# Kernel optimization log

Measured on AMD Instinct MI355X. Metric: run time of the kernel, lower is better.

Reference implementation:

```python
import jax, jax.numpy as jnp
import numpy as np

UNITS = 1024
OMEGA = np.float32(2.0 * np.pi / UNITS)  # Hopf rotation frequency tied to units
MU = np.float32(1.0)                      # bifurcation parameter (the stop-gradient ones)


def _hopf_act(z_prev, z_i):
    # Hopf normal-form activation: z_i + ((mu - |z_i|^2) + i*omega) * z_i
    r2 = z_i.real * z_i.real + z_i.imag * z_i.imag  # float32 [B,U]
    coef = jax.lax.complex(MU - r2, jnp.full_like(r2, OMEGA))
    return z_i + coef * z_i


def setup_inputs() -> dict:
    key = jax.random.key(0)
    ks = jax.random.split(key, 8)
    B, T, U = 64, 512, UNITS
    ws = np.float32(1.0 / np.sqrt(2.0 * U))  # glorot-ish scale for complex weights
    return {
        "x_real": jax.random.normal(ks[0], (B, T, U), dtype=jnp.float32),
        "x_imag": jax.random.normal(ks[1], (B, T, U), dtype=jnp.float32),
        "A_real": jax.random.normal(ks[2], (U, U), dtype=jnp.float32) * ws,
        "A_imag": jax.random.normal(ks[3], (U, U), dtype=jnp.float32) * ws,
        "B_real": jax.random.normal(ks[4], (U, U), dtype=jnp.float32) * ws,
        "B_imag": jax.random.normal(ks[5], (U, U), dtype=jnp.float32) * ws,
        "z0_real": jax.random.normal(ks[6], (B, U), dtype=jnp.float32) * 0.1,
        "z0_imag": jax.random.normal(ks[7], (B, U), dtype=jnp.float32) * 0.1,
    }


def reference(x_real, x_imag, A_real, A_imag, B_real, B_imag, z0_real, z0_imag):
    x = jax.lax.complex(x_real, x_imag)      # [B,T,U] complex64
    A = jax.lax.complex(A_real, A_imag)      # [U,U]
    Bw = jax.lax.complex(B_real, B_imag)     # [U,U]
    z0 = jax.lax.complex(z0_real, z0_imag)   # [B,U]

    def step(z, x_t):
        # z_i = (z @ A + x @ B) / 2 ; new state is z_i, output is Hopf activation
        z_i = (jnp.matmul(z, A) + jnp.matmul(x_t, Bw)) * np.complex64(0.5)
        y_t = _hopf_act(z, z_i)
        return z_i, y_t

    xs = jnp.swapaxes(x, 0, 1)               # [T,B,U]
    _, ys = jax.lax.scan(step, z0, xs)       # ys: [T,B,U]
    ys = jnp.swapaxes(ys, 0, 1)              # [B,T,U]
    # return real/imag stacked so output is float32 [B,T,U,2]
    return jnp.stack([ys.real, ys.imag], axis=-1)
```

## Files before the change

kernel.cpp:

```cpp
#include <hip/hip_runtime.h>
#include <hip/hip_bf16.h>


#define U_DIM 1024
#define T_STEPS 512
#define B_DIM 64
#define CHUNK 16
#define NCH 32
#define R_ROWS 2048

typedef __bf16 bf16;
typedef __attribute__((ext_vector_type(8))) __bf16 bf16x8;
typedef __attribute__((ext_vector_type(4))) float floatx4;
typedef __attribute__((ext_vector_type(8))) float floatx8;
typedef __attribute__((ext_vector_type(2))) float floatx2;
typedef __attribute__((ext_vector_type(4))) int intx4;

static constexpr float OMEGA_F = 0.006135923151542565f;

__global__ __launch_bounds__(256) void wtrans_kernel(
    const float* __restrict__ a0, const float* __restrict__ a1,
    const float* __restrict__ a2, const float* __restrict__ a3,
    bf16* __restrict__ d0, bf16* __restrict__ d1,
    bf16* __restrict__ d2, bf16* __restrict__ d3)
{
  __shared__ bf16 tile[32][33];
  const float* src;
  bf16* dst;
  switch (blockIdx.z) {
    case 0: src = a0; dst = d0; break;
    case 1: src = a1; dst = d1; break;
    case 2: src = a2; dst = d2; break;
    default: src = a3; dst = d3; break;
  }
  const int tx = threadIdx.x;
  const int ty = threadIdx.y;
  const int k0 = blockIdx.x * 32;
  const int n0 = blockIdx.y * 32;
#pragma unroll
  for (int i = 0; i < 4; ++i) {
    int k = k0 + ty + i * 8;
    tile[ty + i * 8][tx] = (bf16)(0.5f * src[(size_t)k * U_DIM + n0 + tx]);
  }
  __syncthreads();
#pragma unroll
  for (int i = 0; i < 4; ++i) {
    int n = n0 + ty + i * 8;
    dst[(size_t)n * U_DIM + k0 + tx] = tile[tx][ty + i * 8];
  }
}

__global__ __launch_bounds__(256) void zinit2_kernel(
    const float* __restrict__ zr, const float* __restrict__ zi,
    bf16* __restrict__ br, bf16* __restrict__ bi)
{
  size_t idx = (size_t)blockIdx.x * 256 + threadIdx.x;
  int row = (int)(idx >> 10);
  int col = (int)(idx & 1023);
  float vr = 0.f, vi = 0.f;
  if (row < 128) {
    int b = row & 63;
    vr = zr[(size_t)b * U_DIM + col];
    vi = zi[(size_t)b * U_DIM + col];
  }
  br[idx] = (bf16)vr;
  bi[idx] = (bf16)vi;
}

__global__ __launch_bounds__(512) void phase1_kernel(
    const float* __restrict__ Xr, const float* __restrict__ Xi,
    const bf16* __restrict__ Wr, const bf16* __restrict__ Wi,
    float* __restrict__ out)
{
  const int lane = threadIdx.x & 63;
  const int wave = threadIdx.x >> 6;
  const int m0 = blockIdx.x * 32;
  const int n0 = blockIdx.y * 512 + wave * 64;
  const int l16 = lane & 15;
  const int kq = (lane >> 4) * 8;

  floatx4 accr[2][4], acci[2][4];
#pragma unroll
  for (int ms = 0; ms < 2; ++ms)
#pragma unroll
    for (int ns = 0; ns < 4; ++ns) {
      accr[ms][ns] = (floatx4){0.f, 0.f, 0.f, 0.f};
      acci[ms][ns] = (floatx4){0.f, 0.f, 0.f, 0.f};
    }

  const float* xr0 = Xr + (size_t)(m0 + l16) * U_DIM + kq;
  const float* xi0 = Xi + (size_t)(m0 + l16) * U_DIM + kq;
  const bf16* wr0 = Wr + (size_t)(n0 + l16) * U_DIM + kq;
  const bf16* wi0 = Wi + (size_t)(n0 + l16) * U_DIM + kq;

#pragma unroll 2
  for (int kb = 0; kb < U_DIM; kb += 32) {
    bf16x8 ar[2], ai[2], nai[2];
#pragma unroll
    for (int ms = 0; ms < 2; ++ms) {
      floatx8 fr = *(const floatx8*)(xr0 + (size_t)ms * 16 * U_DIM + kb);
      floatx8 fi = *(const floatx8*)(xi0 + (size_t)ms * 16 * U_DIM + kb);
      ar[ms] = __builtin_convertvector(fr, bf16x8);
      ai[ms] = __builtin_convertvector(fi, bf16x8);
      intx4 v = __builtin_bit_cast(intx4, ai[ms]);
      v = v ^ (int)0x80008000u;
      nai[ms] = __builtin_bit_cast(bf16x8, v);
    }
    bf16x8 br[4], bi[4];
#pragma unroll
    for (int ns = 0; ns < 4; ++ns) {
      br[ns] = *(const bf16x8*)(wr0 + (size_t)ns * 16 * U_DIM + kb);
      bi[ns] = *(const bf16x8*)(wi0 + (size_t)ns * 16 * U_DIM + kb);
    }
#pragma unroll
    for (int ms = 0; ms < 2; ++ms)
#pragma unroll
      for (int ns = 0; ns < 4; ++ns) {
        accr[ms][ns] = __builtin_amdgcn_mfma_f32_16x16x32_bf16(ar[ms], br[ns], accr[ms][ns], 0, 0, 0);
        accr[ms][ns] = __builtin_amdgcn_mfma_f32_16x16x32_bf16(nai[ms], bi[ns], accr[ms][ns], 0, 0, 0);
        acci[ms][ns] = __builtin_amdgcn_mfma_f32_16x16x32_bf16(ar[ms], bi[ns], acci[ms][ns], 0, 0, 0);
        acci[ms][ns] = __builtin_amdgcn_mfma_f32_16x16x32_bf16(ai[ms], br[ns], acci[ms][ns], 0, 0, 0);
      }
  }

  const int rb = (lane >> 4) * 4;
#pragma unroll
  for (int ms = 0; ms < 2; ++ms)
#pragma unroll
    for (int ns = 0; ns < 4; ++ns)
#pragma unroll
      for (int r = 0; r < 4; ++r) {
        int row = m0 + ms * 16 + rb + r;
        int col = n0 + ns * 16 + l16;
        floatx2 v = {accr[ms][ns][r], acci[ms][ns][r]};
        *(floatx2*)(out + ((size_t)row * U_DIM + col) * 2) = v;
      }
}

__global__ __launch_bounds__(256) void bigstep_kernel(
    const bf16* __restrict__ Zr_in, const bf16* __restrict__ Zi_in,
    const bf16* __restrict__ Wr, const bf16* __restrict__ Wi,
    bf16* __restrict__ Zr_out, bf16* __restrict__ Zi_out,
    float* __restrict__ out, int s, int write_y)
{
  const int lane = threadIdx.x & 63;
  const int wave = threadIdx.x >> 6;
  const int m0 = blockIdx.x * 128 + wave * 32;
  const int n0 = blockIdx.y * 64;
  const int l16 = lane & 15;
  const int kq = (lane >> 4) * 8;

  floatx4 accr[2][4], acci[2][4];
#pragma unroll
  for (int ms = 0; ms < 2; ++ms)
#pragma unroll
    for (int ns = 0; ns < 4; ++ns) {
      accr[ms][ns] = (floatx4){0.f, 0.f, 0.f, 0.f};
      acci[ms][ns] = (floatx4){0.f, 0.f, 0.f, 0.f};
    }

  const bf16* zr0 = Zr_in + (size_t)(m0 + l16) * U_DIM + kq;
  const bf16* zi0 = Zi_in + (size_t)(m0 + l16) * U_DIM + kq;
  const bf16* wr0 = Wr + (size_t)(n0 + l16) * U_DIM + kq;
  const bf16* wi0 = Wi + (size_t)(n0 + l16) * U_DIM + kq;

#pragma unroll 4
  for (int kb = 0; kb < U_DIM; kb += 32) {
    bf16x8 ar[2], ai[2], nai[2];
#pragma unroll
    for (int ms = 0; ms < 2; ++ms) {
      ar[ms] = *(const bf16x8*)(zr0 + (size_t)ms * 16 * U_DIM + kb);
      ai[ms] = *(const bf16x8*)(zi0 + (size_t)ms * 16 * U_DIM + kb);
      intx4 v = __builtin_bit_cast(intx4, ai[ms]);
      v = v ^ (int)0x80008000u;
      nai[ms] = __builtin_bit_cast(bf16x8, v);
    }
    bf16x8 br[4], bi[4];
#pragma unroll
    for (int ns = 0; ns < 4; ++ns) {
      br[ns] = *(const bf16x8*)(wr0 + (size_t)ns * 16 * U_DIM + kb);
      bi[ns] = *(const bf16x8*)(wi0 + (size_t)ns * 16 * U_DIM + kb);
    }
#pragma unroll
    for (int ms = 0; ms < 2; ++ms)
#pragma unroll
      for (int ns = 0; ns < 4; ++ns) {
        accr[ms][ns] = __builtin_amdgcn_mfma_f32_16x16x32_bf16(ar[ms], br[ns], accr[ms][ns], 0, 0, 0);
        accr[ms][ns] = __builtin_amdgcn_mfma_f32_16x16x32_bf16(nai[ms], bi[ns], accr[ms][ns], 0, 0, 0);
        acci[ms][ns] = __builtin_amdgcn_mfma_f32_16x16x32_bf16(ar[ms], bi[ns], acci[ms][ns], 0, 0, 0);
        acci[ms][ns] = __builtin_amdgcn_mfma_f32_16x16x32_bf16(ai[ms], br[ns], acci[ms][ns], 0, 0, 0);
      }
  }

  const int rb = (lane >> 4) * 4;
#pragma unroll
  for (int ms = 0; ms < 2; ++ms)
#pragma unroll
    for (int ns = 0; ns < 4; ++ns)
#pragma unroll
      for (int r = 0; r < 4; ++r) {
        int row = m0 + ms * 16 + rb + r;
        int c = row >> 6;
        int b = row & 63;
        int t = c * CHUNK + s;
        int col = n0 + ns * 16 + l16;
        size_t o = (((size_t)b * T_STEPS + t) * U_DIM + col) * 2;
        floatx2 u = *(const floatx2*)(out + o);
        float zrv = accr[ms][ns][r] + u.x;
        float ziv = acci[ms][ns][r] + u.y;
        Zr_out[(size_t)row * U_DIM + col] = (bf16)zrv;
        Zi_out[(size_t)row * U_DIM + col] = (bf16)ziv;
        if (write_y) {
          float r2 = zrv * zrv + ziv * ziv;
          float cr = 2.0f - r2;
          floatx2 y = {cr * zrv - OMEGA_F * ziv, cr * ziv + OMEGA_F * zrv};
          *(floatx2*)(out + o) = y;
        }
      }
}

extern "C" void kernel_launch(void* const* d_in, const int* in_sizes, int n_in,
                              void* d_out, int out_size, void* d_ws, size_t ws_size,
                              hipStream_t stream)
{
  const float* Xr  = (const float*)d_in[0];
  const float* Xi  = (const float*)d_in[1];
  const float* Ar  = (const float*)d_in[2];
  const float* Ai  = (const float*)d_in[3];
  const float* Br  = (const float*)d_in[4];
  const float* Bi  = (const float*)d_in[5];
  const float* z0r = (const float*)d_in[6];
  const float* z0i = (const float*)d_in[7];
  float* out = (float*)d_out;

  char* ws = (char*)d_ws;
  const size_t WW = (size_t)U_DIM * U_DIM;
  const size_t SB = (size_t)(1 + NCH) * B_DIM * U_DIM;
  const size_t CHOFF = (size_t)B_DIM * U_DIM;
  bf16* Atr = (bf16*)ws;
  bf16* Ati = Atr + WW;
  bf16* Btr = Ati + WW;
  bf16* Bti = Btr + WW;
  bf16* S0r = Bti + WW;
  bf16* S0i = S0r + SB;
  bf16* S1r = S0i + SB;
  bf16* S1i = S1r + SB;

  (void)in_sizes; (void)n_in; (void)out_size; (void)ws_size;

  wtrans_kernel<<<dim3(32, 32, 4), dim3(32, 8), 0, stream>>>(
      Ar, Ai, Br, Bi, Atr, Ati, Btr, Bti);

  zinit2_kernel<<<dim3((unsigned)(SB / 256)), dim3(256), 0, stream>>>(
      z0r, z0i, S0r, S0i);

  phase1_kernel<<<dim3(1024, 2), dim3(512), 0, stream>>>(Xr, Xi, Btr, Bti, out);

  for (int s = 0; s < CHUNK; ++s) {
    const bf16 *ir_, *ii_;
    bf16 *or_, *oi_;
    if ((s & 1) == 0) { ir_ = S0r + CHOFF; ii_ = S0i + CHOFF; or_ = S1r + CHOFF; oi_ = S1i + CHOFF; }
    else              { ir_ = S1r + CHOFF; ii_ = S1i + CHOFF; or_ = S0r + CHOFF; oi_ = S0i + CHOFF; }
    bigstep_kernel<<<dim3(16, 16), dim3(256), 0, stream>>>(
        ir_, ii_, Atr, Ati, or_, oi_, out, s, 0);
  }

  for (int s = 0; s < CHUNK; ++s) {
    const bf16 *ir_, *ii_;
    bf16 *or_, *oi_;
    if (s == 0)       { ir_ = S0r;         ii_ = S0i;         or_ = S1r + CHOFF; oi_ = S1i + CHOFF; }
    else if (s & 1)   { ir_ = S1r + CHOFF; ii_ = S1i + CHOFF; or_ = S0r + CHOFF; oi_ = S0i + CHOFF; }
    else              { ir_ = S0r + CHOFF; ii_ = S0i + CHOFF; or_ = S1r + CHOFF; oi_ = S1i + CHOFF; }
    bigstep_kernel<<<dim3(16, 16), dim3(256), 0, stream>>>(
        ir_, ii_, Atr, Ati, or_, oi_, out, s, 1);
  }
}
```

Baseline: 3.598 ms.

## Tile input-projection GEMM through LDS and split-K the recurrent step kernel

The input projection kernel now stages 128x128 tiles of X (converted to bf16) and W through shared memory with register prefetch of the next K slice, giving each block much more operand reuse than the old per-wave direct global loads. The recurrent step kernel is restructured so the four waves each handle a quarter of K for a 32x64 output tile, with partial sums reduced through LDS by wave 0. This quadruples the grid of each step launch to fill more compute units. The cost is extra LDS traffic, barriers, and a serialized reduction and epilogue on one wave.

```diff
diff --git a/kernel.cpp b/kernel.cpp
--- a/kernel.cpp
+++ b/kernel.cpp
@@ -7,7 +7,6 @@
 #define B_DIM 64
 #define CHUNK 16
 #define NCH 32
-#define R_ROWS 2048
 
 typedef __bf16 bf16;
 typedef __attribute__((ext_vector_type(8))) __bf16 bf16x8;
@@ -67,41 +66,152 @@
   bi[idx] = (bf16)vi;
 }
 
-__global__ __launch_bounds__(512) void phase1_kernel(
+__global__ __launch_bounds__(256, 2) void phase1_kernel(
     const float* __restrict__ Xr, const float* __restrict__ Xi,
     const bf16* __restrict__ Wr, const bf16* __restrict__ Wi,
     float* __restrict__ out)
 {
-  const int lane = threadIdx.x & 63;
-  const int wave = threadIdx.x >> 6;
-  const int m0 = blockIdx.x * 32;
-  const int n0 = blockIdx.y * 512 + wave * 64;
+  __shared__ __align__(16) bf16 ldsA[2][4][128][8];
+  __shared__ __align__(16) bf16 ldsB[2][4][128][8];
+
+  const int t = threadIdx.x;
+  const int lane = t & 63;
+  const int wave = t >> 6;
+  const int wm = wave >> 1;
+  const int wn = wave & 1;
+  const int n0 = blockIdx.x * 128;
+  const int m0 = blockIdx.y * 128;
   const int l16 = lane & 15;
-  const int kq = (lane >> 4) * 8;
-
-  floatx4 accr[2][4], acci[2][4];
-#pragma unroll
-  for (int ms = 0; ms < 2; ++ms)
+  const int kqf = lane >> 4;
+
+  const int sm = t & 127;
+  const int skq = t >> 7;
+
+  floatx4 accr[4][4], acci[4][4];
+#pragma unroll
+  for (int ms = 0; ms < 4; ++ms)
 #pragma unroll
     for (int ns = 0; ns < 4; ++ns) {
       accr[ms][ns] = (floatx4){0.f, 0.f, 0.f, 0.f};
       acci[ms][ns] = (floatx4){0.f, 0.f, 0.f, 0.f};
     }
 
-  const float* xr0 = Xr + (size_t)(m0 + l16) * U_DIM + kq;
-  const float* xi0 = Xi + (size_t)(m0 + l16) * U_DIM + kq;
-  const bf16* wr0 = Wr + (size_t)(n0 + l16) * U_DIM + kq;
-  const bf16* wi0 = Wi + (size_t)(n0 + l16) * U_DIM + kq;
+  const float* xr_base = Xr + (size_t)(m0 + sm) * U_DIM;
+  const float* xi_base = Xi + (size_t)(m0 + sm) * U_DIM;
+  const bf16* wr_base = Wr + (size_t)(n0 + sm) * U_DIM;
+  const bf16* wi_base = Wi + (size_t)(n0 + sm) * U_DIM;
+
+  floatx8 pxr[2], pxi[2];
+  bf16x8 pwr[2], pwi[2];
+
+#define P1_LOADS(KB)                                        \
+  do {                                                      \
+    int ko0 = (KB) + skq * 8;                               \
+    int ko1 = ko0 + 16;                                     \
+    pxr[0] = *(const floatx8*)(xr_base + ko0);              \
+    pxi[0] = *(const floatx8*)(xi_base + ko0);              \
+    pwr[0] = *(const bf16x8*)(wr_base + ko0);               \
+    pwi[0] = *(const bf16x8*)(wi_base + ko0);               \
+    pxr[1] = *(const floatx8*)(xr_base + ko1);              \
+    pxi[1] = *(const floatx8*)(xi_base + ko1);              \
+    pwr[1] = *(const bf16x8*)(wr_base + ko1);               \
+    pwi[1] = *(const bf16x8*)(wi_base + ko1);               \
+  } while (0)
+
+  P1_LOADS(0);
+
+#pragma unroll 1
+  for (int kb = 0; kb < U_DIM; kb += 32) {
+    *(bf16x8*)&ldsA[0][skq][sm][0]     = __builtin_convertvector(pxr[0], bf16x8);
+    *(bf16x8*)&ldsA[1][skq][sm][0]     = __builtin_convertvector(pxi[0], bf16x8);
+    *(bf16x8*)&ldsB[0][skq][sm][0]     = pwr[0];
+    *(bf16x8*)&ldsB[1][skq][sm][0]     = pwi[0];
+    *(bf16x8*)&ldsA[0][skq + 2][sm][0] = __builtin_convertvector(pxr[1], bf16x8);
+    *(bf16x8*)&ldsA[1][skq + 2][sm][0] = __builtin_convertvector(pxi[1], bf16x8);
+    *(bf16x8*)&ldsB[0][skq + 2][sm][0] = pwr[1];
+    *(bf16x8*)&ldsB[1][skq + 2][sm][0] = pwi[1];
+    __syncthreads();
+
+    if (kb + 32 < U_DIM) P1_LOADS(kb + 32);
+
+    bf16x8 br_[4], bi_[4];
+#pragma unroll
+    for (int ns = 0; ns < 4; ++ns) {
+      int nrow = wn * 64 + ns * 16 + l16;
+      br_[ns] = *(const bf16x8*)&ldsB[0][kqf][nrow][0];
+      bi_[ns] = *(const bf16x8*)&ldsB[1][kqf][nrow][0];
+    }
+#pragma unroll
+    for (int ms = 0; ms < 4; ++ms) {
+      int mrow = wm * 64 + ms * 16 + l16;
+      bf16x8 a_r = *(const bf16x8*)&ldsA[0][kqf][mrow][0];
+      bf16x8 a_i = *(const bf16x8*)&ldsA[1][kqf][mrow][0];
+      intx4 v = __builtin_bit_cast(intx4, a_i);
+      v = v ^ (int)0x80008000u;
+      bf16x8 n_ai = __builtin_bit_cast(bf16x8, v);
+#pragma unroll
+      for (int ns = 0; ns < 4; ++ns) {
+        accr[ms][ns] = __builtin_amdgcn_mfma_f32_16x16x32_bf16(a_r,  br_[ns], accr[ms][ns], 0, 0, 0);
+        accr[ms][ns] = __builtin_amdgcn_mfma_f32_16x16x32_bf16(n_ai, bi_[ns], accr[ms][ns], 0, 0, 0);
+        acci[ms][ns] = __builtin_amdgcn_mfma_f32_16x16x32_bf16(a_r,  bi_[ns], acci[ms][ns], 0, 0, 0);
+        acci[ms][ns] = __builtin_amdgcn_mfma_f32_16x16x32_bf16(a_i,  br_[ns], acci[ms][ns], 0, 0, 0);
+      }
+    }
+    __syncthreads();
+  }
+#undef P1_LOADS
+
+  const int rb = (lane >> 4) * 4;
+#pragma unroll
+  for (int ms = 0; ms < 4; ++ms)
+#pragma unroll
+    for (int ns = 0; ns < 4; ++ns)
+#pragma unroll
+      for (int r = 0; r < 4; ++r) {
+        int row = m0 + wm * 64 + ms * 16 + rb + r;
+        int col = n0 + wn * 64 + ns * 16 + l16;
+        floatx2 v = {accr[ms][ns][r], acci[ms][ns][r]};
+        *(floatx2*)(out + ((size_t)row * U_DIM + col) * 2) = v;
+      }
+}
+
+__global__ __launch_bounds__(256, 3) void bigstep_kernel(
+    const bf16* __restrict__ Zr_in, const bf16* __restrict__ Zi_in,
+    const bf16* __restrict__ Wr, const bf16* __restrict__ Wi,
+    bf16* __restrict__ Zr_out, bf16* __restrict__ Zi_out,
+    float* __restrict__ out, int s, int write_y)
+{
+  __shared__ floatx2 hs[3][32 * 64];
+
+  const int lane = threadIdx.x & 63;
+  const int wave = threadIdx.x >> 6;
+  const int n0 = blockIdx.x * 64;
+  const int m0 = blockIdx.y * 32;
+  const int l16 = lane & 15;
+  const int kq = (lane >> 4) * 8;
+  const int kbase = wave * 256;
+
+  floatx4 accr[2][4], acci[2][4];
+#pragma unroll
+  for (int ms = 0; ms < 2; ++ms)
+#pragma unroll
+    for (int ns = 0; ns < 4; ++ns) {
+      accr[ms][ns] = (floatx4){0.f, 0.f, 0.f, 0.f};
+      acci[ms][ns] = (floatx4){0.f, 0.f, 0.f, 0.f};
+    }
+
+  const bf16* zr0 = Zr_in + (size_t)(m0 + l16) * U_DIM + kbase + kq;
+  const bf16* zi0 = Zi_in + (size_t)(m0 + l16) * U_DIM + kbase + kq;
+  const bf16* wr0 = Wr + (size_t)(n0 + l16) * U_DIM + kbase + kq;
+  const bf16* wi0 = Wi + (size_t)(n0 + l16) * U_DIM + kbase + kq;
 
 #pragma unroll 2
-  for (int kb = 0; kb < U_DIM; kb += 32) {
+  for (int kb = 0; kb < 256; kb += 32) {
     bf16x8 ar[2], ai[2], nai[2];
 #pragma unroll
     for (int ms = 0; ms < 2; ++ms) {
-      floatx8 fr = *(const floatx8*)(xr0 + (size_t)ms * 16 * U_DIM + kb);
-      floatx8 fi = *(const floatx8*)(xi0 + (size_t)ms * 16 * U_DIM + kb);
-      ar[ms] = __builtin_convertvector(fr, bf16x8);
-      ai[ms] = __builtin_convertvector(fi, bf16x8);
+      ar[ms] = *(const bf16x8*)(zr0 + (size_t)ms * 16 * U_DIM + kb);
+      ai[ms] = *(const bf16x8*)(zi0 + (size_t)ms * 16 * U_DIM + kb);
       intx4 v = __builtin_bit_cast(intx4, ai[ms]);
       v = v ^ (int)0x80008000u;
       nai[ms] = __builtin_bit_cast(bf16x8, v);
@@ -124,99 +234,51 @@
   }
 
   const int rb = (lane >> 4) * 4;
-#pragma unroll
-  for (int ms = 0; ms < 2; ++ms)
-#pragma unroll
-    for (int ns = 0; ns < 4; ++ns)
-#pragma unroll
-      for (int r = 0; r < 4; ++r) {
-        int row = m0 + ms * 16 + rb + r;
-        int col = n0 + ns * 16 + l16;
-        floatx2 v = {accr[ms][ns][r], acci[ms][ns][r]};
-        *(floatx2*)(out + ((size_t)row * U_DIM + col) * 2) = v;
-      }
-}
-
-__global__ __launch_bounds__(256) void bigstep_kernel(
-    const bf16* __restrict__ Zr_in, const bf16* __restrict__ Zi_in,
-    const bf16* __restrict__ Wr, const bf16* __restrict__ Wi,
-    bf16* __restrict__ Zr_out, bf16* __restrict__ Zi_out,
-    float* __restrict__ out, int s, int write_y)
-{
-  const int lane = threadIdx.x & 63;
-  const int wave = threadIdx.x >> 6;
-  const int m0 = blockIdx.x * 128 + wave * 32;
-  const int n0 = blockIdx.y * 64;
-  const int l16 = lane & 15;
-  const int kq = (lane >> 4) * 8;
-
-  floatx4 accr[2][4], acci[2][4];
-#pragma unroll
-  for (int ms = 0; ms < 2; ++ms)
-#pragma unroll
-    for (int ns = 0; ns < 4; ++ns) {
-      accr[ms][ns] = (floatx4){0.f, 0.f, 0.f, 0.f};
-      acci[ms][ns] = (floatx4){0.f, 0.f, 0.f, 0.f};
-    }
-
-  const bf16* zr0 = Zr_in + (size_t)(m0 + l16) * U_DIM + kq;
-  const bf16* zi0 = Zi_in + (size_t)(m0 + l16) * U_DIM + kq;
-  const bf16* wr0 = Wr + (size_t)(n0 + l16) * U_DIM + kq;
-  const bf16* wi0 = Wi + (size_t)(n0 + l16) * U_DIM + kq;
-
-#pragma unroll 4
-  for (int kb = 0; kb < U_DIM; kb += 32) {
-    bf16x8 ar[2], ai[2], nai[2];
-#pragma unroll
-    for (int ms = 0; ms < 2; ++ms) {
-      ar[ms] = *(const bf16x8*)(zr0 + (size_t)ms * 16 * U_DIM + kb);
-      ai[ms] = *(const bf16x8*)(zi0 + (size_t)ms * 16 * U_DIM + kb);
-      intx4 v = __builtin_bit_cast(intx4, ai[ms]);
-      v = v ^ (int)0x80008000u;
-      nai[ms] = __builtin_bit_cast(bf16x8, v);
-    }
-    bf16x8 br[4], bi[4];
-#pragma unroll
-    for (int ns = 0; ns < 4; ++ns) {
-      br[ns] = *(const bf16x8*)(wr0 + (size_t)ns * 16 * U_DIM + kb);
-      bi[ns] = *(const bf16x8*)(wi0 + (size_t)ns * 16 * U_DIM + kb);
-    }
+  if (wave != 0) {
 #pragma unroll
     for (int ms = 0; ms < 2; ++ms)
 #pragma unroll
-      for (int ns = 0; ns < 4; ++ns) {
-        accr[ms][ns] = __builtin_amdgcn_mfma_f32_16x16x32_bf16(ar[ms], br[ns], accr[ms][ns], 0, 0, 0);
-        accr[ms][ns] = __builtin_amdgcn_mfma_f32_16x16x32_bf16(nai[ms], bi[ns], accr[ms][ns], 0, 0, 0);
-        acci[ms][ns] = __builtin_amdgcn_mfma_f32_16x16x32_bf16(ar[ms], bi[ns], acci[ms][ns], 0, 0, 0);
-        acci[ms][ns] = __builtin_amdgcn_mfma_f32_16x16x32_bf16(ai[ms], br[ns], acci[ms][ns], 0, 0, 0);
-      }
-  }
-
-  const int rb = (lane >> 4) * 4;
-#pragma unroll
-  for (int ms = 0; ms < 2; ++ms)
-#pragma unroll
-    for (int ns = 0; ns < 4; ++ns)
-#pragma unroll
-      for (int r = 0; r < 4; ++r) {
-        int row = m0 + ms * 16 + rb + r;
-        int c = row >> 6;
-        int b = row & 63;
-        int t = c * CHUNK + s;
-        int col = n0 + ns * 16 + l16;
-        size_t o = (((size_t)b * T_STEPS + t) * U_DIM + col) * 2;
-        floatx2 u = *(const floatx2*)(out + o);
-        float zrv = accr[ms][ns][r] + u.x;
-        float ziv = acci[ms][ns][r] + u.y;
-        Zr_out[(size_t)row * U_DIM + col] = (bf16)zrv;
-        Zi_out[(size_t)row * U_DIM + col] = (bf16)ziv;
-        if (write_y) {
-          float r2 = zrv * zrv + ziv * ziv;
-          float cr = 2.0f - r2;
-          floatx2 y = {cr * zrv - OMEGA_F * ziv, cr * ziv + OMEGA_F * zrv};
-          *(floatx2*)(out + o) = y;
+      for (int ns = 0; ns < 4; ++ns)
+#pragma unroll
+        for (int r = 0; r < 4; ++r) {
+          int rl = ms * 16 + rb + r;
+          int cl = ns * 16 + l16;
+          hs[wave - 1][rl * 64 + cl] = (floatx2){accr[ms][ns][r], acci[ms][ns][r]};
         }
-      }
+  }
+  __syncthreads();
+  if (wave == 0) {
+#pragma unroll
+    for (int ms = 0; ms < 2; ++ms)
+#pragma unroll
+      for (int ns = 0; ns < 4; ++ns)
+#pragma unroll
+        for (int r = 0; r < 4; ++r) {
+          int rl = ms * 16 + rb + r;
+          int cl = ns * 16 + l16;
+          int idx = rl * 64 + cl;
+          floatx2 p0 = hs[0][idx];
+          floatx2 p1 = hs[1][idx];
+          floatx2 p2 = hs[2][idx];
+          int row = m0 + rl;
+          int c = row >> 6;
+          int b = row & 63;
+          int tt = c * CHUNK + s;
+          int col = n0 + cl;
+          size_t o = (((size_t)b * T_STEPS + tt) * U_DIM + col) * 2;
+          floatx2 u = *(const floatx2*)(out + o);
+          float zrv = accr[ms][ns][r] + p0.x + p1.x + p2.x + u.x;
+          float ziv = acci[ms][ns][r] + p0.y + p1.y + p2.y + u.y;
+          Zr_out[(size_t)row * U_DIM + col] = (bf16)zrv;
+          Zi_out[(size_t)row * U_DIM + col] = (bf16)ziv;
+          if (write_y) {
+            float r2 = zrv * zrv + ziv * ziv;
+            float cr = 2.0f - r2;
+            floatx2 y = {cr * zrv - OMEGA_F * ziv, cr * ziv + OMEGA_F * zrv};
+            *(floatx2*)(out + o) = y;
+          }
+        }
+  }
 }
 
 extern "C" void kernel_launch(void* const* d_in, const int* in_sizes, int n_in,
@@ -254,14 +316,14 @@
   zinit2_kernel<<<dim3((unsigned)(SB / 256)), dim3(256), 0, stream>>>(
       z0r, z0i, S0r, S0i);
 
-  phase1_kernel<<<dim3(1024, 2), dim3(512), 0, stream>>>(Xr, Xi, Btr, Bti, out);
+  phase1_kernel<<<dim3(8, 256), dim3(256), 0, stream>>>(Xr, Xi, Btr, Bti, out);
 
   for (int s = 0; s < CHUNK; ++s) {
     const bf16 *ir_, *ii_;
     bf16 *or_, *oi_;
     if ((s & 1) == 0) { ir_ = S0r + CHOFF; ii_ = S0i + CHOFF; or_ = S1r + CHOFF; oi_ = S1i + CHOFF; }
     else              { ir_ = S1r + CHOFF; ii_ = S1i + CHOFF; or_ = S0r + CHOFF; oi_ = S0i + CHOFF; }
-    bigstep_kernel<<<dim3(16, 16), dim3(256), 0, stream>>>(
+    bigstep_kernel<<<dim3(16, 64), dim3(256), 0, stream>>>(
         ir_, ii_, Atr, Ati, or_, oi_, out, s, 0);
   }
 
@@ -271,7 +333,7 @@
     if (s == 0)       { ir_ = S0r;         ii_ = S0i;         or_ = S1r + CHOFF; oi_ = S1i + CHOFF; }
     else if (s & 1)   { ir_ = S1r + CHOFF; ii_ = S1i + CHOFF; or_ = S0r + CHOFF; oi_ = S0i + CHOFF; }
     else              { ir_ = S0r + CHOFF; ii_ = S0i + CHOFF; or_ = S1r + CHOFF; oi_ = S1i + CHOFF; }
-    bigstep_kernel<<<dim3(16, 16), dim3(256), 0, stream>>>(
+    bigstep_kernel<<<dim3(16, 64), dim3(256), 0, stream>>>(
         ir_, ii_, Atr, Ati, or_, oi_, out, s, 1);
   }
 }
```

Measured after the change: 3.610 ms. Within noise of the previous version (+0.3%).
